# Kernel tuning notes

Hardware: AMD Instinct MI355X
Metric: run time of the kernel (lower is better)

Reference implementation:

```python
import jax, jax.numpy as jnp
import numpy as np

B, S, H = 2, 2048, 4096
NH, HD = 16, 256          # num heads, head size (H = NH * HD)
RD = 64                   # rotary_dim (GPT-J style partial rotary)
ROPE_BASE = 10000.0
SCALE = HD ** -0.5


def setup_inputs() -> dict:
    key = jax.random.key(0)
    k1, k2, k3 = jax.random.split(key, 3)
    hidden_states = jax.random.normal(k1, (B, S, H), dtype=jnp.float32) * 0.02
    position_ids = jnp.broadcast_to(jnp.arange(S, dtype=jnp.int32), (B, S))
    w_qkv = jax.random.normal(k2, (H, 3 * H), dtype=jnp.float32) * 0.02
    w_out = jax.random.normal(k3, (H, H), dtype=jnp.float32) * 0.02
    return {"hidden_states": hidden_states, "position_ids": position_ids,
            "w_qkv": w_qkv, "w_out": w_out}


def _rope_gptj(x, positions):
    # x: [B, S, NH, HD]; GPT-J interleaved (non-neox) RoPE on first RD dims
    inv_freq = 1.0 / (ROPE_BASE ** (jnp.arange(0, RD, 2, dtype=jnp.float32) / RD))
    freqs = positions.astype(jnp.float32)[..., None] * inv_freq   # [B,S,RD/2]
    cos = jnp.cos(freqs)[:, :, None, :]                            # [B,S,1,RD/2]
    sin = jnp.sin(freqs)[:, :, None, :]
    x_rot, x_pass = x[..., :RD], x[..., RD:]
    x1, x2 = x_rot[..., 0::2], x_rot[..., 1::2]                    # interleaved pairs
    o1 = x1 * cos - x2 * sin
    o2 = x2 * cos + x1 * sin
    rot = jnp.stack([o1, o2], axis=-1).reshape(x_rot.shape)        # re-interleave
    return jnp.concatenate([rot, x_pass], axis=-1)


def reference(hidden_states, position_ids, w_qkv, w_out):
    # fused QKV projection; note Moss splits as q, v, k
    qkv = jnp.einsum('bsh,hf->bsf', hidden_states, w_qkv)
    q, v, k = jnp.split(qkv, 3, axis=-1)
    q = q.reshape(B, S, NH, HD)
    k = k.reshape(B, S, NH, HD)
    v = v.reshape(B, S, NH, HD)
    q = _rope_gptj(q, position_ids)
    k = _rope_gptj(k, position_ids)
    # causal scaled dot-product attention
    scores = jnp.einsum('bqhd,bkhd->bhqk', q, k) * SCALE           # [B,NH,S,S]
    causal = jnp.tril(jnp.ones((S, S), dtype=bool))
    scores = jnp.where(causal, scores, jnp.finfo(scores.dtype).min)
    probs = jax.nn.softmax(scores, axis=-1)
    attn = jnp.einsum('bhqk,bkhd->bqhd', probs, v).reshape(B, S, H)
    return jnp.einsum('bsh,ho->bso', attn, w_out)
```

## Files before the change

kernel.cpp:

```cpp
#include <hip/hip_runtime.h>
#include <hip/hip_bf16.h>
#include <cmath>

#define B_ 2
#define S_ 2048
#define H_ 4096
#define NH_ 16
#define HD_ 256
#define RD_ 64
#define F3_ 12288
#define TOK_ (B_*S_)

static constexpr float SCALE_ = 0.0625f;

typedef __bf16 bf16;
typedef bf16 bf16x8 __attribute__((ext_vector_type(8)));
typedef bf16 bf16x4 __attribute__((ext_vector_type(4)));
typedef float f32x4 __attribute__((ext_vector_type(4)));

union BU2 { unsigned int u; bf16 h[2]; };

__global__ void k_hcvt(const float* __restrict__ in, bf16* __restrict__ out, int n8) {
  int i = blockIdx.x * 256 + threadIdx.x;
  if (i >= n8) return;
  const float4* p = (const float4*)in + (size_t)i * 2;
  float4 a = p[0], b = p[1];
  bf16x8 v;
  v[0] = (bf16)a.x; v[1] = (bf16)a.y; v[2] = (bf16)a.z; v[3] = (bf16)a.w;
  v[4] = (bf16)b.x; v[5] = (bf16)b.y; v[6] = (bf16)b.z; v[7] = (bf16)b.w;
  ((bf16x8*)out)[i] = v;
}

__global__ void k_tcvt(const float* __restrict__ in, bf16* __restrict__ out, int R, int C) {
  __shared__ float tile[32][33];
  int c0 = blockIdx.x * 32, r0 = blockIdx.y * 32;
  int x = threadIdx.x, y = threadIdx.y;
#pragma unroll
  for (int k = 0; k < 4; ++k)
    tile[y + 8 * k][x] = in[(size_t)(r0 + y + 8 * k) * C + c0 + x];
  __syncthreads();
#pragma unroll
  for (int k = 0; k < 4; ++k)
    out[(size_t)(c0 + y + 8 * k) * R + r0 + x] = (bf16)tile[x][y + 8 * k];
}

__global__ void k_rope_table(float* __restrict__ cosT, float* __restrict__ sinT) {
  int pos = blockIdx.x, j = threadIdx.x;
  float invf = (float)pow(10000.0, -2.0 * (double)j / 64.0);
  float ang = (float)pos * invf;
  cosT[pos * 32 + j] = cosf(ang);
  sinT[pos * 32 + j] = sinf(ang);
}

__global__ void k_rope_reorder(const bf16* __restrict__ qkv, const int* __restrict__ pid,
                               const float* __restrict__ cosT, const float* __restrict__ sinT,
                               bf16* __restrict__ Qo, bf16* __restrict__ Ko) {
  int tok = blockIdx.x;
  int b = tok >> 11, s = tok & (S_ - 1);
  int t = threadIdx.x;
  int hh = t >> 7, tt = t & 127;
  int pos = pid[tok];
  int d = tt * 2;
  float c = 1.f, sn = 0.f;
  if (tt < 32) { c = cosT[pos * 32 + tt]; sn = sinT[pos * 32 + tt]; }
#pragma unroll
  for (int hs = 0; hs < 8; ++hs) {
    int h = hs * 2 + hh;
    size_t iq = (size_t)tok * F3_ + h * HD_ + d;
    size_t oo = ((size_t)(b * NH_ + h) * S_ + s) * HD_ + d;
    BU2 q; q.u = *(const unsigned int*)(qkv + iq);
    BU2 k; k.u = *(const unsigned int*)(qkv + iq + 2 * H_);
    BU2 qo, ko;
    if (tt < 32) {
      float q1 = (float)q.h[0], q2 = (float)q.h[1];
      float k1 = (float)k.h[0], k2 = (float)k.h[1];
      qo.h[0] = (bf16)(q1 * c - q2 * sn); qo.h[1] = (bf16)(q2 * c + q1 * sn);
      ko.h[0] = (bf16)(k1 * c - k2 * sn); ko.h[1] = (bf16)(k2 * c + k1 * sn);
    } else { qo = q; ko = k; }
    *(unsigned int*)(Qo + oo) = qo.u;
    *(unsigned int*)(Ko + oo) = ko.u;
  }
}

__global__ void k_vtrans(const bf16* __restrict__ qkv, bf16* __restrict__ VT) {
  __shared__ float tile[64][129];
  int bid = blockIdx.x;
  int st = bid & 31, bh = bid >> 5;
  int b = bh >> 4, h = bh & 15;
  int t = threadIdx.x;
  for (int half = 0; half < 2; ++half) {
#pragma unroll
    for (int r = 0; r < 16; ++r) {
      int i = r * 4 + (t >> 6);
      int d = (t & 63) * 2;
      int s = st * 64 + i;
      size_t idx = (size_t)(b * S_ + s) * F3_ + H_ + h * HD_ + half * 128 + d;
      BU2 v; v.u = *(const unsigned int*)(qkv + idx);
      tile[i][d] = (float)v.h[0];
      tile[i][d + 1] = (float)v.h[1];
    }
    __syncthreads();
    int i = t & 63, dg = t >> 6;
    size_t ob = ((size_t)bh * HD_ + half * 128) * S_ + st * 64 + i;
#pragma unroll
    for (int dd = 0; dd < 32; ++dd) {
      int dcol = dd * 4 + dg;
      VT[ob + (size_t)dcol * S_] = (bf16)tile[i][dcol];
    }
    __syncthreads();
  }
}


#define GK_ 4096

#define STG(dst, half, src, row0, k0)                                                     \
  do {                                                                                    \
    const bf16* _s0 = (src) + (size_t)((row0) + (half) * 128 + sr0) * GK_ + (k0) + sc0;   \
    const bf16* _s1 = (src) + (size_t)((row0) + (half) * 128 + sr1) * GK_ + (k0) + sc1;   \
    __builtin_amdgcn_global_load_lds(                                                     \
        (const __attribute__((address_space(1))) void*)_s0,                               \
        (__attribute__((address_space(3))) void*)((char*)(dst) + (half) * 16384 + so0),   \
        16, 0, 0);                                                                        \
    __builtin_amdgcn_global_load_lds(                                                     \
        (const __attribute__((address_space(1))) void*)_s1,                               \
        (__attribute__((address_space(3))) void*)((char*)(dst) + (half) * 16384 + so1),   \
        16, 0, 0);                                                                        \
  } while (0)

#define LDA(buf, mh)                                                                      \
  _Pragma("unroll") for (int mt = 0; mt < 4; ++mt)                                        \
  _Pragma("unroll") for (int kk = 0; kk < 2; ++kk)                                        \
    aF[mt][kk] = *(const bf16x8*)((const char*)(buf) + aBase + ((mh)*4 + mt) * 2048 + kk * 64);

#define LDB(dst, buf, nh)                                                                 \
  _Pragma("unroll") for (int nt = 0; nt < 2; ++nt)                                        \
  _Pragma("unroll") for (int kk = 0; kk < 2; ++kk)                                        \
    dst[nt][kk] = *(const bf16x8*)((const char*)(buf) + bBase + ((nh)*2 + nt) * 2048 + kk * 64);

#define MM(mh, nh, bfrag)                                                                 \
  _Pragma("unroll") for (int mt = 0; mt < 4; ++mt)                                        \
  _Pragma("unroll") for (int nt = 0; nt < 2; ++nt)                                        \
  _Pragma("unroll") for (int kk = 0; kk < 2; ++kk)                                        \
    acc[(mh)*4 + mt][(nh)*2 + nt] = __builtin_amdgcn_mfma_f32_16x16x32_bf16(              \
        aF[mt][kk], bfrag[nt][kk], acc[(mh)*4 + mt][(nh)*2 + nt], 0, 0, 0);

#define BAR __builtin_amdgcn_s_barrier()
#define LGKM0 asm volatile("s_waitcnt lgkmcnt(0)" ::: "memory")
#define VMW4 asm volatile("s_waitcnt vmcnt(4)" ::: "memory")
#define VMW0 asm volatile("s_waitcnt vmcnt(0)" ::: "memory")
#define PRIO1 __builtin_amdgcn_s_setprio(1)
#define PRIO0 __builtin_amdgcn_s_setprio(0)

template <bool OUT_F32>
__global__ __launch_bounds__(512, 1)
void k_gemm8(const bf16* __restrict__ A, const bf16* __restrict__ BT,
             void* __restrict__ Cv, int Nn, int gx) {
  __shared__ bf16 As0[256 * 64];
  __shared__ bf16 As1[256 * 64];
  __shared__ bf16 Bs0[256 * 64];
  __shared__ bf16 Bs1[256 * 64];

  int nwg = gridDim.x;
  int bid = blockIdx.x;
  int q = nwg >> 3, r = nwg & 7;
  int xcd = bid & 7, lid = bid >> 3;
  int wg = (xcd < r ? xcd * (q + 1) : r * (q + 1) + (xcd - r) * q) + lid;
  int bx = wg % gx, by = wg / gx;
  int m0 = by * 256, n0 = bx * 256;

  int tid = threadIdx.x;
  int lane = tid & 63, w = tid >> 6;
  int wr = w >> 2, wc = w & 3;
  int lrow = lane & 15, g = lane >> 4;
  int sig = (lrow >> 2) & 1;
  int cswz = (g * 16) ^ (sig << 5);
  int aBase = (wr * 128 + lrow) * 128 + cswz;
  int bBase = (wc * 64 + lrow) * 128 + cswz;

  int ci0 = w * 64 + lane;
  int ci1 = 512 + ci0;
  int sr0 = ci0 >> 3, sr1 = ci1 >> 3;
  int sc0 = ((ci0 & 7) ^ (((ci0 >> 5) & 1) << 1)) * 8;
  int sc1 = ((ci1 & 7) ^ (((ci1 >> 5) & 1) << 1)) * 8;
  int so0 = ci0 * 16, so1 = ci1 * 16;

  STG(As0, 0, A, m0, 0);
  STG(As0, 1, A, m0, 0);
  STG(Bs0, 0, BT, n0, 0);
  STG(Bs0, 1, BT, n0, 0);
  STG(Bs1, 0, BT, n0, 64);
  STG(Bs1, 1, BT, n0, 64);

  const f32x4 Z4 = {0.f, 0.f, 0.f, 0.f};
  f32x4 acc[8][4];
#pragma unroll
  for (int i = 0; i < 8; ++i)
#pragma unroll
    for (int jj = 0; jj < 4; ++jj) acc[i][jj] = Z4;

  bf16x8 aF[4][2], bFa[2][2], bFb[2][2];

  VMW4;
  BAR;

  const int NIT = GK_ / 128;
  for (int j = 0; j < NIT; ++j) {
    bool last = (j == NIT - 1);
    int kT1 = (2 * j + 1) * 64;
    int kT2 = (2 * j + 2) * 64;
    int kT3 = (2 * j + 3) * 64;
    LDA(As0, 0); LDB(bFa, Bs0, 0);
    STG(As1, 0, A, m0, kT1);
    BAR; LGKM0; PRIO1; MM(0, 0, bFa); PRIO0; BAR;
    LDB(bFb, Bs0, 1);
    STG(As1, 1, A, m0, kT1);
    BAR; LGKM0; PRIO1; MM(0, 1, bFb); PRIO0; BAR;
    LDA(As0, 1);
    if (!last) STG(Bs0, 0, BT, n0, kT2);
    BAR; LGKM0; PRIO1; MM(1, 1, bFb); PRIO0; BAR;
    if (!last) { STG(Bs0, 1, BT, n0, kT2); VMW4; } else { VMW0; }
    BAR; PRIO1; MM(1, 0, bFa); PRIO0; BAR;
    LDA(As1, 0); LDB(bFa, Bs1, 0);
    if (!last) STG(As0, 0, A, m0, kT2);
    BAR; LGKM0; PRIO1; MM(0, 0, bFa); PRIO0; BAR;
    LDB(bFb, Bs1, 1);
    if (!last) STG(As0, 1, A, m0, kT2);
    BAR; LGKM0; PRIO1; MM(0, 1, bFb); PRIO0; BAR;
    LDA(As1, 1);
    if (!last) STG(Bs1, 0, BT, n0, kT3);
    BAR; LGKM0; PRIO1; MM(1, 1, bFb); PRIO0; BAR;
    if (!last) { STG(Bs1, 1, BT, n0, kT3); VMW4; }
    BAR; PRIO1; MM(1, 0, bFa); PRIO0; BAR;
  }

#pragma unroll
  for (int mt = 0; mt < 8; ++mt)
#pragma unroll
    for (int nt = 0; nt < 4; ++nt)
#pragma unroll
      for (int rr = 0; rr < 4; ++rr) {
        int m = m0 + wr * 128 + mt * 16 + g * 4 + rr;
        int n = n0 + wc * 64 + nt * 16 + lrow;
        if (OUT_F32)
          ((float*)Cv)[(size_t)m * Nn + n] = acc[mt][nt][rr];
        else
          ((bf16*)Cv)[(size_t)m * Nn + n] = (bf16)acc[mt][nt][rr];
      }
}

__global__ __launch_bounds__(256, 2)
void k_attn(const bf16* __restrict__ Q, const bf16* __restrict__ K,
            const bf16* __restrict__ VT, bf16* __restrict__ O) {
  __shared__ bf16 Ks[64 * 256];
  __shared__ bf16 Vs[256 * 64];
  __shared__ bf16 Ps[4][16 * 80];

  int qt = blockIdx.x;
  int bh = blockIdx.y;
  int tid = threadIdx.x;
  int lane = tid & 63, wv = tid >> 6;

  int qrow = qt * 64 + wv * 16 + (lane & 15);
  const bf16* Qb = Q + ((size_t)bh * S_ + qrow) * HD_;
  bf16x8 qf[8];
#pragma unroll
  for (int dc = 0; dc < 8; ++dc)
    qf[dc] = *(const bf16x8*)(Qb + dc * 32 + (lane >> 4) * 8);

  const f32x4 Z4 = {0.f, 0.f, 0.f, 0.f};
  f32x4 o[16];
#pragma unroll
  for (int i = 0; i < 16; ++i) o[i] = Z4;
  float m_i[4], l_i[4];
#pragma unroll
  for (int r = 0; r < 4; ++r) { m_i[r] = -INFINITY; l_i[r] = 0.f; }

  const bf16* Kb = K + (size_t)bh * S_ * HD_;
  const bf16* Vb = VT + (size_t)bh * HD_ * S_;

  for (int t = 0; t <= qt; ++t) {
    int kv0 = t * 64;
    {
      int i0 = tid >> 5;
      int doff = (tid & 31) * 8;
#pragma unroll
      for (int it = 0; it < 8; ++it) {
        int row = it * 8 + i0;
        bf16x8 gld = *(const bf16x8*)(Kb + (size_t)(kv0 + row) * HD_ + doff);
        int el = (row * 256 + doff) ^ ((row & 7) << 3);
        *(bf16x8*)&Ks[el] = gld;
      }
      int d0 = tid >> 3;
      int koff = (tid & 7) * 8;
#pragma unroll
      for (int it = 0; it < 8; ++it) {
        int dr = it * 32 + d0;
        bf16x8 gld = *(const bf16x8*)(Vb + (size_t)dr * S_ + kv0 + koff);
        int el = (dr * 64 + koff) ^ ((dr & 7) << 3);
        *(bf16x8*)&Vs[el] = gld;
      }
    }
    __syncthreads();

    f32x4 sa[4];
#pragma unroll
    for (int nt = 0; nt < 4; ++nt) sa[nt] = Z4;
#pragma unroll
    for (int dc = 0; dc < 8; ++dc)
#pragma unroll
      for (int nt = 0; nt < 4; ++nt) {
        int kvr = nt * 16 + (lane & 15);
        int el = (kvr * 256 + dc * 32 + (lane >> 4) * 8) ^ ((kvr & 7) << 3);
        sa[nt] = __builtin_amdgcn_mfma_f32_16x16x32_bf16(qf[dc], *(const bf16x8*)&Ks[el], sa[nt], 0, 0, 0);
      }

    float p[4][4], mx[4];
    bool diag = (t == qt);
#pragma unroll
    for (int r = 0; r < 4; ++r) {
      float vmax = -INFINITY;
#pragma unroll
      for (int nt = 0; nt < 4; ++nt) {
        float v = sa[nt][r] * SCALE_;
        if (diag) {
          int q_abs = qt * 64 + wv * 16 + (lane >> 4) * 4 + r;
          int kv_abs = kv0 + nt * 16 + (lane & 15);
          if (kv_abs > q_abs) v = -1e30f;
        }
        p[nt][r] = v;
        vmax = fmaxf(vmax, v);
      }
      mx[r] = vmax;
    }
#pragma unroll
    for (int off = 1; off < 16; off <<= 1)
#pragma unroll
      for (int r = 0; r < 4; ++r) mx[r] = fmaxf(mx[r], __shfl_xor(mx[r], off));
    float sf[4], rs[4];
#pragma unroll
    for (int r = 0; r < 4; ++r) {
      float mnew = fmaxf(m_i[r], mx[r]);
      sf[r] = __expf(m_i[r] - mnew);
      float sum = 0.f;
#pragma unroll
      for (int nt = 0; nt < 4; ++nt) {
        p[nt][r] = __expf(p[nt][r] - mnew);
        sum += p[nt][r];
      }
      rs[r] = sum;
      m_i[r] = mnew;
    }
#pragma unroll
    for (int off = 1; off < 16; off <<= 1)
#pragma unroll
      for (int r = 0; r < 4; ++r) rs[r] += __shfl_xor(rs[r], off);
#pragma unroll
    for (int r = 0; r < 4; ++r) l_i[r] = l_i[r] * sf[r] + rs[r];
#pragma unroll
    for (int dt = 0; dt < 16; ++dt)
#pragma unroll
      for (int r = 0; r < 4; ++r) o[dt][r] *= sf[r];

#pragma unroll
    for (int nt = 0; nt < 4; ++nt)
#pragma unroll
      for (int r = 0; r < 4; ++r)
        Ps[wv][((lane >> 4) * 4 + r) * 80 + nt * 16 + (lane & 15)] = (bf16)p[nt][r];

#pragma unroll
    for (int kc = 0; kc < 2; ++kc) {
      bf16x8 pf = *(const bf16x8*)&Ps[wv][(lane & 15) * 80 + kc * 32 + (lane >> 4) * 8];
#pragma unroll
      for (int dt = 0; dt < 16; ++dt) {
        int drow = dt * 16 + (lane & 15);
        int el = (drow * 64 + kc * 32 + (lane >> 4) * 8) ^ ((drow & 7) << 3);
        o[dt] = __builtin_amdgcn_mfma_f32_16x16x32_bf16(pf, *(const bf16x8*)&Vs[el], o[dt], 0, 0, 0);
      }
    }
    __syncthreads();
  }

  int b = bh >> 4, h = bh & 15;
  float inv[4];
#pragma unroll
  for (int r = 0; r < 4; ++r) inv[r] = 1.0f / l_i[r];
#pragma unroll
  for (int dt = 0; dt < 16; ++dt)
#pragma unroll
    for (int r = 0; r < 4; ++r) {
      int q_abs = qt * 64 + wv * 16 + (lane >> 4) * 4 + r;
      O[((size_t)(b * S_ + q_abs)) * H_ + h * HD_ + dt * 16 + (lane & 15)] = (bf16)(o[dt][r] * inv[r]);
    }
}

extern "C" void kernel_launch(void* const* d_in, const int* in_sizes, int n_in,
                              void* d_out, int out_size, void* d_ws, size_t ws_size,
                              hipStream_t stream) {
  const float* hidden = (const float*)d_in[0];
  const int* pid = (const int*)d_in[1];
  const float* wqkv = (const float*)d_in[2];
  const float* wout = (const float*)d_in[3];
  float* outp = (float*)d_out;
  char* ws = (char*)d_ws;

  const size_t OFF_WQT = 0;
  const size_t OFF_WOT = OFF_WQT + (size_t)F3_ * H_ * 2;
  const size_t OFF_QKV = OFF_WOT + (size_t)H_ * H_ * 2;
  const size_t OFF_O = OFF_QKV;
  const size_t OFF_Q = OFF_QKV + (size_t)TOK_ * F3_ * 2;
  const size_t OFF_K = OFF_Q + (size_t)TOK_ * H_ * 2;
  const size_t OFF_VT = OFF_K + (size_t)TOK_ * H_ * 2;
  const size_t OFF_COS = OFF_VT + (size_t)TOK_ * H_ * 2;
  const size_t OFF_SIN = OFF_COS + (size_t)S_ * 32 * 4;
  const size_t TOTAL = OFF_SIN + (size_t)S_ * 32 * 4;
  if (ws_size < TOTAL) return;

  bf16* WqT = (bf16*)(ws + OFF_WQT);
  bf16* WoT = (bf16*)(ws + OFF_WOT);
  bf16* qkv = (bf16*)(ws + OFF_QKV);
  bf16* Obuf = (bf16*)(ws + OFF_O);
  bf16* Qb = (bf16*)(ws + OFF_Q);
  bf16* Kb = (bf16*)(ws + OFF_K);
  bf16* VTb = (bf16*)(ws + OFF_VT);
  float* cosT = (float*)(ws + OFF_COS);
  float* sinT = (float*)(ws + OFF_SIN);
  bf16* HB = (bf16*)(ws + OFF_Q);

  k_tcvt<<<dim3(F3_ / 32, H_ / 32), dim3(32, 8), 0, stream>>>(wqkv, WqT, H_, F3_);
  k_tcvt<<<dim3(H_ / 32, H_ / 32), dim3(32, 8), 0, stream>>>(wout, WoT, H_, H_);
  k_rope_table<<<dim3(S_), dim3(32), 0, stream>>>(cosT, sinT);
  k_hcvt<<<dim3(TOK_ * H_ / 8 / 256), dim3(256), 0, stream>>>(hidden, HB, TOK_ * H_ / 8);
  k_gemm8<false><<<dim3((F3_ / 256) * (TOK_ / 256)), dim3(512), 0, stream>>>(
      HB, WqT, qkv, F3_, F3_ / 256);
  k_rope_reorder<<<dim3(TOK_), dim3(256), 0, stream>>>(qkv, pid, cosT, sinT, Qb, Kb);
  k_vtrans<<<dim3(B_ * NH_ * (S_ / 64)), dim3(256), 0, stream>>>(qkv, VTb);
  k_attn<<<dim3(S_ / 64, B_ * NH_), dim3(256), 0, stream>>>(Qb, Kb, VTb, Obuf);
  k_gemm8<true><<<dim3((H_ / 256) * (TOK_ / 256)), dim3(512), 0, stream>>>(
      Obuf, WoT, outp, H_, H_ / 256);
}
```

Measured before the change: 1.561 ms.

## Read K/V fragments directly from global memory in attention, drop LDS staging

The attention kernel no longer stages K and V tiles in shared memory with block-wide barriers. Each wave now loads its MFMA operand fragments straight from global memory, relying on L1/L2 caching since all four waves read the same K/V. With the 64 KB of shared memory gone, the occupancy hint rises to 4 blocks per CU. Query tiles are launched in reverse order so the longest causal tiles start first. The risk is extra global and cache traffic, with each wave fetching K/V separately, and exposed load latency in front of every MFMA.

After: 2.400 ms. +53.8%, slower.

```diff
diff --git a/kernel.cpp b/kernel.cpp
--- a/kernel.cpp
+++ b/kernel.cpp
@@ -249,24 +249,23 @@
       }
 }
 
-__global__ __launch_bounds__(256, 2)
+__global__ __launch_bounds__(256, 4)
 void k_attn(const bf16* __restrict__ Q, const bf16* __restrict__ K,
             const bf16* __restrict__ VT, bf16* __restrict__ O) {
-  __shared__ bf16 Ks[64 * 256];
-  __shared__ bf16 Vs[256 * 64];
   __shared__ bf16 Ps[4][16 * 80];
 
-  int qt = blockIdx.x;
+  int qt = gridDim.x - 1 - blockIdx.x;
   int bh = blockIdx.y;
   int tid = threadIdx.x;
   int lane = tid & 63, wv = tid >> 6;
-
-  int qrow = qt * 64 + wv * 16 + (lane & 15);
+  int lrow = lane & 15, g = lane >> 4;
+
+  int qrow = qt * 64 + wv * 16 + lrow;
   const bf16* Qb = Q + ((size_t)bh * S_ + qrow) * HD_;
   bf16x8 qf[8];
 #pragma unroll
   for (int dc = 0; dc < 8; ++dc)
-    qf[dc] = *(const bf16x8*)(Qb + dc * 32 + (lane >> 4) * 8);
+    qf[dc] = *(const bf16x8*)(Qb + dc * 32 + g * 8);
 
   const f32x4 Z4 = {0.f, 0.f, 0.f, 0.f};
   f32x4 o[16];
@@ -281,27 +280,6 @@
 
   for (int t = 0; t <= qt; ++t) {
     int kv0 = t * 64;
-    {
-      int i0 = tid >> 5;
-      int doff = (tid & 31) * 8;
-#pragma unroll
-      for (int it = 0; it < 8; ++it) {
-        int row = it * 8 + i0;
-        bf16x8 gld = *(const bf16x8*)(Kb + (size_t)(kv0 + row) * HD_ + doff);
-        int el = (row * 256 + doff) ^ ((row & 7) << 3);
-        *(bf16x8*)&Ks[el] = gld;
-      }
-      int d0 = tid >> 3;
-      int koff = (tid & 7) * 8;
-#pragma unroll
-      for (int it = 0; it < 8; ++it) {
-        int dr = it * 32 + d0;
-        bf16x8 gld = *(const bf16x8*)(Vb + (size_t)dr * S_ + kv0 + koff);
-        int el = (dr * 64 + koff) ^ ((dr & 7) << 3);
-        *(bf16x8*)&Vs[el] = gld;
-      }
-    }
-    __syncthreads();
 
     f32x4 sa[4];
 #pragma unroll
@@ -310,9 +288,8 @@
     for (int dc = 0; dc < 8; ++dc)
 #pragma unroll
       for (int nt = 0; nt < 4; ++nt) {
-        int kvr = nt * 16 + (lane & 15);
-        int el = (kvr * 256 + dc * 32 + (lane >> 4) * 8) ^ ((kvr & 7) << 3);
-        sa[nt] = __builtin_amdgcn_mfma_f32_16x16x32_bf16(qf[dc], *(const bf16x8*)&Ks[el], sa[nt], 0, 0, 0);
+        bf16x8 kf = *(const bf16x8*)(Kb + (size_t)(kv0 + nt * 16 + lrow) * HD_ + dc * 32 + g * 8);
+        sa[nt] = __builtin_amdgcn_mfma_f32_16x16x32_bf16(qf[dc], kf, sa[nt], 0, 0, 0);
       }
 
     float p[4][4], mx[4];
@@ -324,8 +301,8 @@
       for (int nt = 0; nt < 4; ++nt) {
         float v = sa[nt][r] * SCALE_;
         if (diag) {
-          int q_abs = qt * 64 + wv * 16 + (lane >> 4) * 4 + r;
-          int kv_abs = kv0 + nt * 16 + (lane & 15);
+          int q_abs = qt * 64 + wv * 16 + g * 4 + r;
+          int kv_abs = kv0 + nt * 16 + lrow;
           if (kv_abs > q_abs) v = -1e30f;
         }
         p[nt][r] = v;
@@ -366,19 +343,17 @@
     for (int nt = 0; nt < 4; ++nt)
 #pragma unroll
       for (int r = 0; r < 4; ++r)
-        Ps[wv][((lane >> 4) * 4 + r) * 80 + nt * 16 + (lane & 15)] = (bf16)p[nt][r];
+        Ps[wv][(g * 4 + r) * 80 + nt * 16 + lrow] = (bf16)p[nt][r];
 
 #pragma unroll
     for (int kc = 0; kc < 2; ++kc) {
-      bf16x8 pf = *(const bf16x8*)&Ps[wv][(lane & 15) * 80 + kc * 32 + (lane >> 4) * 8];
+      bf16x8 pf = *(const bf16x8*)&Ps[wv][lrow * 80 + kc * 32 + g * 8];
 #pragma unroll
       for (int dt = 0; dt < 16; ++dt) {
-        int drow = dt * 16 + (lane & 15);
-        int el = (drow * 64 + kc * 32 + (lane >> 4) * 8) ^ ((drow & 7) << 3);
-        o[dt] = __builtin_amdgcn_mfma_f32_16x16x32_bf16(pf, *(const bf16x8*)&Vs[el], o[dt], 0, 0, 0);
+        bf16x8 vf = *(const bf16x8*)(Vb + (size_t)(dt * 16 + lrow) * S_ + kv0 + kc * 32 + g * 8);
+        o[dt] = __builtin_amdgcn_mfma_f32_16x16x32_bf16(pf, vf, o[dt], 0, 0, 0);
       }
     }
-    __syncthreads();
   }
 
   int b = bh >> 4, h = bh & 15;
@@ -389,8 +364,8 @@
   for (int dt = 0; dt < 16; ++dt)
 #pragma unroll
     for (int r = 0; r < 4; ++r) {
-      int q_abs = qt * 64 + wv * 16 + (lane >> 4) * 4 + r;
-      O[((size_t)(b * S_ + q_abs)) * H_ + h * HD_ + dt * 16 + (lane & 15)] = (bf16)(o[dt][r] * inv[r]);
+      int q_abs = qt * 64 + wv * 16 + g * 4 + r;
+      O[((size_t)(b * S_ + q_abs)) * H_ + h * HD_ + dt * 16 + lrow] = (bf16)(o[dt][r] * inv[r]);
     }
 }
 
```
